# Optimization experiments

Measured on AMD Instinct MI355X. Metric: run time of the kernel, lower is better.

The kernel has to match this reference:

```python
import jax, jax.numpy as jnp
import numpy as np

K = 8            # hard-coded knn k
NS = 0.2         # LeakyReLU negative slope
EPS = 1e-6
LN_EPS = 1e-5
H = 6            # num_heads


def vn_lin(W, x):
    # VNLinear: linear over vector-channel dim (axis 1). x: (B, Cin, 3, ...)
    return jnp.einsum('oc,bc...->bo...', W, x)


def vn_leaky(x, W, U):
    # VNLinearLeakyReLU (no BN): feature map p, direction map d
    p = vn_lin(W, x)
    d = vn_lin(U, x)
    dot = jnp.sum(p * d, axis=2, keepdims=True)
    dsq = jnp.sum(d * d, axis=2, keepdims=True)
    neg = p - (dot / (dsq + EPS)) * d
    return NS * p + (1.0 - NS) * jnp.where(dot >= 0, p, neg)


def vn_layernorm(x, g, b):
    # LayerNorm on per-channel vector norms, rescale directions. x: (B,C,3,N)
    n = jnp.sqrt(jnp.sum(x * x, axis=2) + EPS)            # (B,C,N)
    mu = jnp.mean(n, axis=1, keepdims=True)
    var = jnp.var(n, axis=1, keepdims=True)
    nhat = (n - mu) / jnp.sqrt(var + LN_EPS)
    nnew = g[None, :, None] * nhat + b[None, :, None]
    return x * (nnew / n)[:, :, None, :]


def vn_attention(vn_x, Wq, Wk, Wv, Wo):
    # vn_x: (B, C, 3, N); VNLinear(C, 3C) projections, multi-head SDPA over N
    B, C, _, N = vn_x.shape
    def heads(W):
        t = vn_lin(W, vn_x)                               # (B, 3C, 3, N)
        t = t.reshape(B, H, 3 * C // H, 3, N)
        return t.transpose(0, 1, 4, 2, 3).reshape(B, H, N, -1)  # (B,H,N,9C/H)
    q, k, v = heads(Wq), heads(Wk), heads(Wv)
    scale = (3 * C // H) ** -0.5                          # head_dim = dim//H = 64
    attn = jax.nn.softmax(jnp.einsum('bhqd,bhkd->bhqk', q, k) * scale, axis=-1)
    o = jnp.einsum('bhqk,bhkd->bhqd', attn, v)            # (B,H,N,9C/H)
    o = o.transpose(0, 2, 1, 3).reshape(B, N, 3 * C, 3).transpose(0, 2, 3, 1)
    return vn_lin(Wo, o)                                  # (B, C, 3, N)


def vn_get_graph_feature(x, knn_index):
    # x: (B, C, 3, N); knn_index: flat (B*K*N,) into (B*N) rows
    B, C, _, N = x.shape
    xp = x.transpose(0, 3, 1, 2).reshape(B * N, C * 3)
    feat = xp[knn_index].reshape(B, K, N, C, 3)
    xc = x.transpose(0, 3, 1, 2).reshape(B, 1, N, C, 3)
    f = jnp.concatenate([feat - xc, jnp.broadcast_to(xc, (B, K, N, C, 3))], axis=3)
    return f.transpose(0, 3, 4, 2, 1)                     # (B, 2C, 3, N, K)


def setup_inputs() -> dict:
    key = jax.random.key(0)
    ks = jax.random.split(key, 20)
    B, N, C = 4, 2048, 128
    def w(k, o, i):
        return jax.random.normal(k, (o, i), jnp.float32) * (i ** -0.5)
    return {
        'x': jax.random.normal(ks[0], (B, N, 3 * C), jnp.float32),
        'knn_index': jax.random.randint(ks[1], (B * K * N,), 0, B * N),
        'g1': jnp.ones((C,), jnp.float32), 'b1': jnp.zeros((C,), jnp.float32),
        'g2': jnp.ones((C,), jnp.float32), 'b2': jnp.zeros((C,), jnp.float32),
        'Wq': w(ks[2], 3 * C, C), 'Wk': w(ks[3], 3 * C, C), 'Wv': w(ks[4], 3 * C, C),
        'Wo': w(ks[5], C, 3 * C),
        'W1': w(ks[6], C, 2 * C), 'U1': w(ks[7], C, 2 * C),   # conv1: 256->128
        'W2': w(ks[8], C, 2 * C),                               # conv2: 256->128
        'W3': w(ks[9], 2 * C, C), 'U3': w(ks[10], 2 * C, C),   # conv3: 128->256
        'W4': w(ks[11], C, 2 * C), 'U4': w(ks[12], C, 2 * C),  # conv4: 256->128
    }


def reference(x, knn_index, g1, b1, g2, b2, Wq, Wk, Wv, Wo, W1, U1, W2, W3, U3, W4, U4):
    B, N, D = x.shape
    C = D // 3
    vn_x = x.transpose(0, 2, 1).reshape(B, C, 3, N)
    norm_x = vn_layernorm(vn_x, g1, b1)
    x_1 = vn_attention(norm_x, Wq, Wk, Wv, Wo)            # (B,C,3,N)
    knn_f = vn_get_graph_feature(norm_x, knn_index)       # (B,2C,3,N,K)
    knn_f = vn_leaky(knn_f, W1, U1)                       # (B,C,3,N,K)
    knn_f = jnp.mean(knn_f, axis=-1)                      # mean_pool over k
    x_1 = jnp.concatenate([x_1, knn_f], axis=1)           # (B,2C,3,N)
    x_1 = vn_lin(W2, x_1)                                 # (B,C,3,N)
    vn_x = vn_x + x_1
    nx2 = vn_layernorm(vn_x, g2, b2)
    h = vn_leaky(nx2, W3, U3)                             # (B,2C,3,N)
    h = vn_leaky(h, W4, U4)                               # (B,C,3,N)
    vn_x = vn_x + h
    return vn_x.reshape(B, D, N).transpose(0, 2, 1)       # (B,N,384)
```

## Files before the change

kernel.cpp:

```cpp
#include <hip/hip_runtime.h>
#include <math.h>

#define NFIX 2048
#define HH 6
#define KNN 8
#define NSLOPE 0.2f
#define EPSF 1e-6f
#define LNEPSF 1e-5f
#define QSCALE 0.18033688011112042f
#define NSPLIT 2

typedef unsigned short ushort_t;
typedef unsigned int uint_t;
typedef __attribute__((ext_vector_type(8))) short bf16x8;
typedef __attribute__((ext_vector_type(4))) short bf16x4;
typedef __attribute__((ext_vector_type(8))) _Float16 f16x8;
typedef __attribute__((ext_vector_type(4))) _Float16 f16x4;
typedef __attribute__((ext_vector_type(16))) float f32x16;
typedef __attribute__((ext_vector_type(4))) float f32x4;

__device__ __forceinline__ ushort_t f2bf(float f) {
  union { float f; unsigned u; } v; v.f = f;
  unsigned r = v.u + 0x7fff + ((v.u >> 16) & 1);
  return (ushort_t)(r >> 16);
}
__device__ __forceinline__ float bf2f(ushort_t u) {
  union { uint_t u; float f; } v; v.u = ((uint_t)u) << 16; return v.f;
}
__device__ __forceinline__ uint_t pack2(float a, float b) {
  return (uint_t)f2bf(a) | ((uint_t)f2bf(b) << 16);
}
__device__ __forceinline__ ushort_t f2h_bits(float a) {
  union { _Float16 h; ushort_t s; } cv; cv.h = (_Float16)a; return cv.s;
}
__device__ __forceinline__ uint_t packh2(float a, float b) {
  union { _Float16 h; ushort_t s; } ha, hb;
  ha.h = (_Float16)a; hb.h = (_Float16)b;
  return (uint_t)ha.s | ((uint_t)hb.s << 16);
}

__device__ __forceinline__ void vnleaky3(const float* p, const float* dv, float* out) {
  float dot = p[0]*dv[0] + p[1]*dv[1] + p[2]*dv[2];
  float dsq = dv[0]*dv[0] + dv[1]*dv[1] + dv[2]*dv[2] + EPSF;
  float f = dot / dsq;
#pragma unroll
  for (int d = 0; d < 3; ++d) {
    float neg = p[d] - f * dv[d];
    out[d] = NSLOPE * p[d] + (1.f - NSLOPE) * ((dot >= 0.f) ? p[d] : neg);
  }
}

__global__ __launch_bounds__(256) void prep_ln1(
    const float* __restrict__ Wq, const float* __restrict__ Wk,
    const float* __restrict__ Wv, const float* __restrict__ Wo,
    const float* __restrict__ W1, const float* __restrict__ U1,
    const float* __restrict__ W2, const float* __restrict__ W3,
    const float* __restrict__ U3, const float* __restrict__ W4,
    const float* __restrict__ U4,
    ushort_t* __restrict__ Wall, _Float16* __restrict__ Af16,
    _Float16* __restrict__ W3h, _Float16* __restrict__ U3h,
    _Float16* __restrict__ W4h, _Float16* __restrict__ U4h,
    const float* __restrict__ xin, ushort_t* __restrict__ xbp,
    float* __restrict__ xdi, const float* __restrict__ g1,
    const float* __restrict__ b1) {
  __shared__ float red[8];
  int bi = blockIdx.x;
  if (bi >= 1600) {
    int t = threadIdx.x;
    int half = t >> 7, c = t & 127;
    int bn = (bi - 1600) * 2 + half;
    const float* row = xin + (size_t)bn * 384;
    float x0 = row[c*3+0], x1 = row[c*3+1], x2 = row[c*3+2];
    float nv = sqrtf(x0*x0 + x1*x1 + x2*x2 + EPSF);
    float s1 = nv, s2 = nv*nv;
#pragma unroll
    for (int off = 32; off >= 1; off >>= 1) {
      s1 += __shfl_down(s1, off);
      s2 += __shfl_down(s2, off);
    }
    int lane = t & 63, w = t >> 6;
    if (lane == 0) { red[w*2] = s1; red[w*2+1] = s2; }
    __syncthreads();
    int rb4 = (w >> 1) * 4;
    float tot1 = red[rb4] + red[rb4+2], tot2 = red[rb4+1] + red[rb4+3];
    float mu  = tot1 * (1.f/128.f);
    float var = tot2 * (1.f/128.f) - mu*mu;
    float rsig = rsqrtf(var + LNEPSF);
    float nnew = g1[c] * ((nv - mu) * rsig) + b1[c];
    float sc = nnew / nv;
    size_t rb = (size_t)bn * 384;
    xbp[rb + c]       = f2bf(x0*sc);
    xbp[rb + 128 + c] = f2bf(x1*sc);
    xbp[rb + 256 + c] = f2bf(x2*sc);
    xdi[rb + c]       = x0;
    xdi[rb + 128 + c] = x1;
    xdi[rb + 256 + c] = x2;
    return;
  }
  int idx = bi * 256 + threadIdx.x;
  if (idx < 212992) {
    int m = idx >> 7, c = idx & 127;
    float val;
    if (m < 384)       val = Wq[m*128 + c] * QSCALE;
    else if (m < 768)  val = Wk[(m-384)*128 + c];
    else if (m < 1152) val = Wv[(m-768)*128 + c];
    else {
      int j = m - 1152;
      if (j < 128)      val = W1[j*256 + c];
      else if (j < 256) val = U1[(j-128)*256 + c];
      else if (j < 384) { int o = j-256; val = W1[o*256 + 128 + c] - W1[o*256 + c]; }
      else              { int o = j-384; val = U1[o*256 + 128 + c] - U1[o*256 + c]; }
    }
    Wall[idx] = f2bf(val); return;
  }
  idx -= 212992;
  if (idx < 49152) {
    int c = idx / 384, j = idx % 384;
    float s = 0.f;
    for (int cp = 0; cp < 128; ++cp) s += W2[c*256 + cp] * Wo[cp*384 + j];
    Af16[(size_t)c*512 + j] = (_Float16)s; return;
  }
  idx -= 49152;
  if (idx < 16384) {
    int c2 = idx / 128, c = idx % 128;
    Af16[(size_t)c*512 + 384 + c2] = (_Float16)W2[c*256 + 128 + c2]; return;
  }
  idx -= 16384;
  if (idx < 32768) { W3h[idx] = (_Float16)W3[idx]; return; }
  idx -= 32768;
  if (idx < 32768) { U3h[idx] = (_Float16)U3[idx]; return; }
  idx -= 32768;
  if (idx < 32768) { W4h[idx] = (_Float16)W4[idx]; return; }
  idx -= 32768;
  if (idx < 32768) { U4h[idx] = (_Float16)U4[idx]; return; }
}

#define XT_PITCH 132
#define WT_PITCH 132
#define TR_PITCH 36
__global__ __launch_bounds__(256, 2) void qkv_conv1_mfma(
    const ushort_t* __restrict__ xb, const ushort_t* __restrict__ Wall,
    ushort_t* __restrict__ q, ushort_t* __restrict__ k, ushort_t* __restrict__ v,
    _Float16* __restrict__ YZh, _Float16* __restrict__ NBh) {
  __shared__ ushort_t xs[128*XT_PITCH];
  __shared__ ushort_t wt[32*WT_PITCH];
  __shared__ float tr[4][32*TR_PITCH];
  int nb = blockIdx.x % 192;
  int mq = blockIdx.x / 192;
  int n0 = nb * 128;
  int t = threadIdx.x;
  int w = t >> 6, lane = t & 63, ql = lane & 31, hl = lane >> 5;
  for (int idx = t; idx < 2048; idx += 256) {
    int n = idx >> 4, c16 = idx & 15;
    bf16x8 gv = *(const bf16x8*)&xb[(size_t)(n0 + n)*128 + c16*8];
    ushort_t* dst = &xs[n*XT_PITCH + c16*8];
    *(bf16x4*)dst = __builtin_shufflevector(gv, gv, 0, 1, 2, 3);
    *(bf16x4*)(dst+4) = __builtin_shufflevector(gv, gv, 4, 5, 6, 7);
  }
  __syncthreads();
  bf16x8 xf[8];
  {
    const ushort_t* xr = &xs[(w*32 + ql)*XT_PITCH + hl*8];
#pragma unroll
    for (int cs = 0; cs < 8; ++cs) {
      bf16x4 lo = *(const bf16x4*)(xr + cs*16);
      bf16x4 hi = *(const bf16x4*)(xr + cs*16 + 4);
      xf[cs] = __builtin_shufflevector(lo, hi, 0, 1, 2, 3, 4, 5, 6, 7);
    }
  }
  int ng = n0 + w*32 + ql;
  int pt = ng / 3;
  int d  = ng - 3*pt;
  float* trw = tr[w];
  for (int mt = 0; mt < 13; ++mt) {
    int m0 = mq*416 + mt*32;
    __syncthreads();
    for (int idx = t; idx < 512; idx += 256) {
      int mm = idx >> 4, c16 = idx & 15;
      bf16x8 gv = *(const bf16x8*)&Wall[(size_t)(m0 + mm)*128 + c16*8];
      ushort_t* dst = &wt[mm*WT_PITCH + c16*8];
      *(bf16x4*)dst = __builtin_shufflevector(gv, gv, 0, 1, 2, 3);
      *(bf16x4*)(dst+4) = __builtin_shufflevector(gv, gv, 4, 5, 6, 7);
    }
    __syncthreads();
    f32x16 acc;
#pragma unroll
    for (int r = 0; r < 16; ++r) acc[r] = 0.f;
    const ushort_t* wr = &wt[ql*WT_PITCH + hl*8];
#pragma unroll
    for (int cs = 0; cs < 8; ++cs) {
      bf16x4 lo = *(const bf16x4*)(wr + cs*16);
      bf16x4 hi = *(const bf16x4*)(wr + cs*16 + 4);
      bf16x8 af = __builtin_shufflevector(lo, hi, 0, 1, 2, 3, 4, 5, 6, 7);
      acc = __builtin_amdgcn_mfma_f32_32x32x16_bf16(af, xf[cs], acc, 0, 0, 0);
    }
#pragma unroll
    for (int r = 0; r < 16; ++r) {
      int mrow = (r&3) + 8*(r>>2) + 4*hl;
      trw[ql*TR_PITCH + mrow] = acc[r];
    }
    asm volatile("s_waitcnt lgkmcnt(0)" ::: "memory");
    float4 c0 = *(float4*)&trw[ql*TR_PITCH + hl*16 + 0];
    float4 c1 = *(float4*)&trw[ql*TR_PITCH + hl*16 + 4];
    float4 c2 = *(float4*)&trw[ql*TR_PITCH + hl*16 + 8];
    float4 c3 = *(float4*)&trw[ql*TR_PITCH + hl*16 + 12];
    asm volatile("s_waitcnt lgkmcnt(0)" ::: "memory");
    int mg = m0 + hl*16;
    if (m0 < 1152) {
      uint4 s0, s1;
      s0.x = pack2(c0.x, c0.y); s0.y = pack2(c0.z, c0.w);
      s0.z = pack2(c1.x, c1.y); s0.w = pack2(c1.z, c1.w);
      s1.x = pack2(c2.x, c2.y); s1.y = pack2(c2.z, c2.w);
      s1.z = pack2(c3.x, c3.y); s1.w = pack2(c3.z, c3.w);
      ushort_t* dst;
      if (m0 < 384)       dst = q + (size_t)pt*1152 + d*384 + mg;
      else if (m0 < 768)  dst = k + (size_t)pt*1152 + d*384 + (mg - 384);
      else                dst = v + (size_t)pt*1152 + d*384 + (mg - 768);
      *(uint4*)dst = s0;
      *(uint4*)(dst + 8) = s1;
    } else {
      int mat = mg - 1152;
      int sub = mat >> 7, o = mat & 127;
      _Float16* basep = (sub < 2) ? YZh : NBh;
      _Float16* dst = basep + (size_t)pt*768 + d*256 + (sub & 1)*128 + o;
      uint4 s0, s1;
      s0.x = packh2(c0.x, c0.y); s0.y = packh2(c0.z, c0.w);
      s0.z = packh2(c1.x, c1.y); s0.w = packh2(c1.z, c1.w);
      s1.x = packh2(c2.x, c2.y); s1.y = packh2(c2.z, c2.w);
      s1.z = packh2(c3.x, c3.y); s1.w = packh2(c3.z, c3.w);
      *(uint4*)dst = s0;
      *(uint4*)(dst + 8) = s1;
    }
  }
}

#define VT_LP 196
__global__ __launch_bounds__(256) void post_vtrans(const ushort_t* __restrict__ v,
    ushort_t* __restrict__ vT, const _Float16* __restrict__ YZh,
    const _Float16* __restrict__ NBh, const int* __restrict__ knn_index,
    _Float16* __restrict__ kmf16) {
  __shared__ ushort_t tl[64*VT_LP];
  __shared__ int sidx[8][KNN];
  int blk = blockIdx.x;
  int t = threadIdx.x;
  if (blk < 768) {
    int bh = blk / 32, ptile = blk % 32;
    int b = bh / HH, h = bh % HH;
    int pt0 = ptile * 64;
#pragma unroll
    for (int i = 0; i < 6; ++i) {
      int u = i*256 + t;
      int p = u / 24, seg = u % 24;
      int d = seg >> 3, c8 = seg & 7;
      bf16x8 gv = *(const bf16x8*)&v[(size_t)(b*NFIX + pt0 + p)*1152 + d*384 + h*64 + c8*8];
      ushort_t* dst = &tl[p*VT_LP + d*64 + c8*8];
      *(bf16x4*)dst = __builtin_shufflevector(gv, gv, 0, 1, 2, 3);
      *(bf16x4*)(dst+4) = __builtin_shufflevector(gv, gv, 4, 5, 6, 7);
    }
    __syncthreads();
#pragma unroll
    for (int i = 0; i < 6; ++i) {
      int u = i*256 + t;
      int ch = u >> 3, pc = u & 7;
      int ol = ch / 3, dd = ch - 3*ol;
      int cloc = dd*64 + ol;
      ushort_t hv[8];
#pragma unroll
      for (int e = 0; e < 8; ++e)
        hv[e] = tl[(pc*8 + e)*VT_LP + cloc];
      uint4 o4;
      o4.x = (uint_t)hv[0] | ((uint_t)hv[1] << 16);
      o4.y = (uint_t)hv[2] | ((uint_t)hv[3] << 16);
      o4.z = (uint_t)hv[4] | ((uint_t)hv[5] << 16);
      o4.w = (uint_t)hv[6] | ((uint_t)hv[7] << 16);
      *(uint4*)&vT[((size_t)bh*192 + ch)*2048 + pt0 + pc*8] = o4;
    }
    return;
  }
  int bnb = (blk - 768) * 8;
  int half = t >> 7, c = t & 127;
  if (t < 64) {
    int pi = t >> 3, kk = t & 7;
    int bn = bnb + pi;
    int b = bn / NFIX, n = bn % NFIX;
    sidx[pi][kk] = knn_index[(b*KNN + kk)*NFIX + n];
  }
  __syncthreads();
#pragma unroll
  for (int pi2 = 0; pi2 < 4; ++pi2) {
    int pi = half*4 + pi2;
    int bn = bnb + pi;
    float yb[3], zb[3];
#pragma unroll
    for (int d = 0; d < 3; ++d) {
      yb[d] = (float)NBh[(size_t)bn*768 + d*256 + c];
      zb[d] = (float)NBh[(size_t)bn*768 + d*256 + 128 + c];
    }
    float om[3] = {0.f, 0.f, 0.f};
#pragma unroll
    for (int kk = 0; kk < KNN; ++kk) {
      const _Float16* r = YZh + (size_t)sidx[pi][kk]*768;
      float p[3], dd[3];
#pragma unroll
      for (int d = 0; d < 3; ++d) {
        p[d]  = (float)r[d*256 + c] + yb[d];
        dd[d] = (float)r[d*256 + 128 + c] + zb[d];
      }
      float res[3];
      vnleaky3(p, dd, res);
      om[0] += res[0]; om[1] += res[1]; om[2] += res[2];
    }
#pragma unroll
    for (int d = 0; d < 3; ++d)
      kmf16[((size_t)bn*3 + d)*128 + c] = (_Float16)(om[d] * (1.f/KNN));
  }
}

#define KT_P 196
#define VT_P 36
#define TW_P 195
__global__ __launch_bounds__(256, 2) void attn_kernel(const ushort_t* __restrict__ q,
    const ushort_t* __restrict__ k, const ushort_t* __restrict__ vT,
    ushort_t* __restrict__ opart, float* __restrict__ lpart) {
  __shared__ ushort_t kt[2][32*KT_P];
  __shared__ ushort_t vt[2][192*VT_P];
  __shared__ float alds[4][32];
  int blk = blockIdx.x;
  int xcd = blk & 7, j = blk >> 3;
  int g = xcd*6 + (j >> 4);
  int qt = j & 15;
  int bh = g % 24;
  int split = g / 24;
  int b = bh / HH, h = bh % HH;
  int t = threadIdx.x;
  int w = t >> 6, lane = t & 63, ql = lane & 31, hl = lane >> 5;
  int qrow0 = qt*128 + w*32;
  const ushort_t* qpb = q + (size_t)(b*NFIX + qrow0 + ql)*1152 + h*64;
  bf16x8 qf[12];
#pragma unroll
  for (int cs = 0; cs < 12; ++cs) {
    int red0 = cs*16 + hl*8;
    int dq = red0 >> 6, ml = red0 & 63;
    qf[cs] = *(const bf16x8*)(qpb + dq*384 + ml);
  }
  const ushort_t* ksrc[3]; int kdsto[3];
  const ushort_t* vsrc[3]; int vdsto[3];
#pragma unroll
  for (int j2 = 0; j2 < 3; ++j2) {
    int idx = t + j2*256;
    int kp = idx / 24, c16 = idx % 24;
    int red0 = c16*8;
    int dk = red0 >> 6, ml = red0 & 63;
    ksrc[j2] = k + (size_t)(b*NFIX + kp)*1152 + dk*384 + h*64 + ml;
    kdsto[j2] = kp*KT_P + c16*8;
    int ch = idx >> 2, c4 = idx & 3;
    vsrc[j2] = vT + ((size_t)bh*192 + ch)*2048 + c4*8;
    vdsto[j2] = ch*VT_P + c4*8;
  }
  f32x16 acc[6];
#pragma unroll
  for (int nt = 0; nt < 6; ++nt)
#pragma unroll
    for (int r = 0; r < 16; ++r) acc[nt][r] = 0.f;
  float lsum = 0.f;
  int koff0 = split * 1024;
  bf16x8 kpre[3], vpre[3];
#pragma unroll
  for (int j2 = 0; j2 < 3; ++j2) {
    kpre[j2] = *(const bf16x8*)(ksrc[j2] + (size_t)koff0*1152);
    vpre[j2] = *(const bf16x8*)(vsrc[j2] + koff0);
  }
#pragma unroll
  for (int j2 = 0; j2 < 3; ++j2) {
    ushort_t* kd = &kt[0][kdsto[j2]];
    *(bf16x4*)kd = __builtin_shufflevector(kpre[j2], kpre[j2], 0, 1, 2, 3);
    *(bf16x4*)(kd+4) = __builtin_shufflevector(kpre[j2], kpre[j2], 4, 5, 6, 7);
    ushort_t* vd = &vt[0][vdsto[j2]];
    *(bf16x4*)vd = __builtin_shufflevector(vpre[j2], vpre[j2], 0, 1, 2, 3);
    *(bf16x4*)(vd+4) = __builtin_shufflevector(vpre[j2], vpre[j2], 4, 5, 6, 7);
  }
  __syncthreads();
  for (int kb = 0; kb < 32; ++kb) {
    int cur = kb & 1;
    if (kb < 31) {
      int koff = koff0 + (kb+1)*32;
#pragma unroll
      for (int j2 = 0; j2 < 3; ++j2) {
        kpre[j2] = *(const bf16x8*)(ksrc[j2] + (size_t)koff*1152);
        vpre[j2] = *(const bf16x8*)(vsrc[j2] + koff);
      }
    }
    f32x16 sca, scb;
#pragma unroll
    for (int r = 0; r < 16; ++r) { sca[r] = 0.f; scb[r] = 0.f; }
    const ushort_t* ktc = kt[cur];
#pragma unroll
    for (int cs = 0; cs < 12; ++cs) {
      const ushort_t* kr = &ktc[ql*KT_P + cs*16 + hl*8];
      bf16x4 alo = *(const bf16x4*)kr;
      bf16x4 ahi = *(const bf16x4*)(kr + 4);
      bf16x8 af = __builtin_shufflevector(alo, ahi, 0, 1, 2, 3, 4, 5, 6, 7);
      if (cs & 1) scb = __builtin_amdgcn_mfma_f32_32x32x16_bf16(af, qf[cs], scb, 0, 0, 0);
      else        sca = __builtin_amdgcn_mfma_f32_32x32x16_bf16(af, qf[cs], sca, 0, 0, 0);
    }
    uint_t u[8], pex[8];
#pragma unroll
    for (int g2 = 0; g2 < 4; ++g2) {
      float p0 = __builtin_amdgcn_exp2f(sca[g2*4 + 0] + scb[g2*4 + 0]);
      float p1 = __builtin_amdgcn_exp2f(sca[g2*4 + 1] + scb[g2*4 + 1]);
      float p2 = __builtin_amdgcn_exp2f(sca[g2*4 + 2] + scb[g2*4 + 2]);
      float p3 = __builtin_amdgcn_exp2f(sca[g2*4 + 3] + scb[g2*4 + 3]);
      lsum += (p0 + p1) + (p2 + p3);
      u[2*g2]   = pack2(p0, p1);
      u[2*g2+1] = pack2(p2, p3);
    }
#pragma unroll
    for (int j2 = 0; j2 < 8; ++j2) pex[j2] = (uint_t)__shfl_xor((int)u[j2], 32);
    const ushort_t* vtc = vt[cur];
#pragma unroll
    for (int s = 0; s < 2; ++s) {
      uint4 au;
      au.x = hl ? pex[4*s+2] : u[4*s+0];
      au.y = hl ? pex[4*s+3] : u[4*s+1];
      au.z = hl ? u[4*s+2]   : pex[4*s+0];
      au.w = hl ? u[4*s+3]   : pex[4*s+1];
      union { uint4 ui; bf16x8 bv; } cvt; cvt.ui = au;
      bf16x8 pa = cvt.bv;
#pragma unroll
      for (int nt = 0; nt < 6; ++nt) {
        const ushort_t* vr = &vtc[(nt*32 + ql)*VT_P + s*16 + hl*8];
        bf16x4 vlo = *(const bf16x4*)vr;
        bf16x4 vhi = *(const bf16x4*)(vr + 4);
        bf16x8 vf = __builtin_shufflevector(vlo, vhi, 0, 1, 2, 3, 4, 5, 6, 7);
        acc[nt] = __builtin_amdgcn_mfma_f32_32x32x16_bf16(pa, vf, acc[nt], 0, 0, 0);
      }
    }
    if (kb < 31) {
      int nxt = cur ^ 1;
#pragma unroll
      for (int j2 = 0; j2 < 3; ++j2) {
        ushort_t* kd = &kt[nxt][kdsto[j2]];
        *(bf16x4*)kd = __builtin_shufflevector(kpre[j2], kpre[j2], 0, 1, 2, 3);
        *(bf16x4*)(kd+4) = __builtin_shufflevector(kpre[j2], kpre[j2], 4, 5, 6, 7);
        ushort_t* vd = &vt[nxt][vdsto[j2]];
        *(bf16x4*)vd = __builtin_shufflevector(vpre[j2], vpre[j2], 0, 1, 2, 3);
        *(bf16x4*)(vd+4) = __builtin_shufflevector(vpre[j2], vpre[j2], 4, 5, 6, 7);
      }
    }
    __syncthreads();
  }
  lsum += __shfl_xor(lsum, 32);
  if (lane < 32) {
    alds[w][ql] = 1.0f / lsum;
    lpart[(size_t)split*24*NFIX + (size_t)bh*NFIX + qrow0 + ql] = lsum;
  }
  asm volatile("s_waitcnt lgkmcnt(0)" ::: "memory");
  float lv[4][4];
#pragma unroll
  for (int g2 = 0; g2 < 4; ++g2) {
    f32x4 tv = *(const f32x4*)&alds[w][8*g2 + 4*hl];
#pragma unroll
    for (int rr = 0; rr < 4; ++rr) lv[g2][rr] = tv[rr];
  }
  ushort_t* tw = (w == 0) ? kt[0] : (w == 1) ? kt[1] : (w == 2) ? vt[0] : vt[1];
#pragma unroll
  for (int nt = 0; nt < 6; ++nt) {
    int ch = nt*32 + ql;
#pragma unroll
    for (int r = 0; r < 16; ++r) {
      int qrow = (r&3) + 8*(r>>2) + 4*hl;
      tw[qrow*TW_P + ch] = f2h_bits(acc[nt][r] * lv[r>>2][r&3]);
    }
  }
  asm volatile("s_waitcnt lgkmcnt(0)" ::: "memory");
  const size_t SS = (size_t)8192*1152;
  ushort_t* opb = opart + (size_t)split*SS;
  size_t nbase = (size_t)(b*NFIX + qrow0) * 3;
#pragma unroll
  for (int i = 0; i < 12; ++i) {
    int chunk = i*64 + lane;
    int nl = chunk >> 3, jc = chunk & 7;
    int qq = nl / 3, dd = nl - 3*qq;
    ushort_t hv[8];
#pragma unroll
    for (int e = 0; e < 8; ++e)
      hv[e] = tw[qq*TW_P + (jc*8 + e)*3 + dd];
    uint4 sv;
    sv.x = (uint_t)hv[0] | ((uint_t)hv[1] << 16);
    sv.y = (uint_t)hv[2] | ((uint_t)hv[3] << 16);
    sv.z = (uint_t)hv[4] | ((uint_t)hv[5] << 16);
    sv.w = (uint_t)hv[6] | ((uint_t)hv[7] << 16);
    *(uint4*)&opb[(nbase + nl)*384 + h*64 + jc*8] = sv;
  }
}

#define AP 68
#define XLP 132
__global__ __launch_bounds__(768) void x1mid_mfma(
    const float* __restrict__ xdi, const ushort_t* __restrict__ opart,
    const float* __restrict__ lpart, const _Float16* __restrict__ kmf16,
    const _Float16* __restrict__ Af16, float* __restrict__ xmid,
    _Float16* __restrict__ nxh, const float* __restrict__ g2,
    const float* __restrict__ b2) {
  __shared__ __align__(16) char smem[50944];
  _Float16* As = (_Float16*)smem;
  _Float16* Bt = (_Float16*)(smem + 17408);
  float* wlsL  = (float*)(smem + 30464);
  float* X     = (float*)smem;
  float* stats = (float*)(smem + 50688);
  int blk = blockIdx.x;
  int n0 = blk * 96;
  int pt0 = blk * 32;
  int t = threadIdx.x;
  int w = t >> 6, lane = t & 63, ql = lane & 31, hl = lane >> 5;
  int nsub = w >> 2, mt2 = w & 3;
  if (t < 192) {
    int ptl = t / 6, h = t % 6;
    int ptg = pt0 + ptl;
    int b = ptg >> 11, n = ptg & 2047;
    size_t lidx = (size_t)(b*HH + h)*NFIX + n;
    float l[NSPLIT]; float tot = 0.f;
#pragma unroll
    for (int s = 0; s < NSPLIT; ++s) {
      l[s] = lpart[(size_t)s*24*NFIX + lidx];
      tot += l[s];
    }
    float rd = 1.f / tot;
    float* wp = &wlsL[(ptl*6 + h)*NSPLIT];
#pragma unroll
    for (int s = 0; s < NSPLIT; ++s) wp[s] = l[s]*rd;
  }
  f32x16 acc;
#pragma unroll
  for (int r = 0; r < 16; ++r) acc[r] = 0.f;
  const size_t SS = (size_t)8192*1152;
  __syncthreads();
  for (int p = 0; p < 8; ++p) {
    for (int u = t; u < 1024; u += 768) {
      int m = u >> 3, kc = u & 7;
      f16x4 a0 = *(const f16x4*)&Af16[(size_t)m*512 + p*64 + kc*8];
      f16x4 a1 = *(const f16x4*)&Af16[(size_t)m*512 + p*64 + kc*8 + 4];
      _Float16* dst = &As[m*AP + kc*8];
      *(f16x4*)dst = a0;
      *(f16x4*)(dst+4) = a1;
    }
    {
      int n_l = t >> 3, jc = t & 7;
      int n_g = n0 + n_l;
      _Float16* dst = &Bt[n_l*AP + jc*8];
      if (p < 6) {
        int pt_l = n_l / 3;
        const float* wp = &wlsL[(pt_l*6 + p)*NSPLIT];
        float facc[8];
#pragma unroll
        for (int e = 0; e < 8; ++e) facc[e] = 0.f;
#pragma unroll
        for (int s = 0; s < NSPLIT; ++s) {
          const ushort_t* src = opart + s*SS + (size_t)n_g*384 + p*64 + jc*8;
          uint4 ra = *(const uint4*)src;
          const _Float16* ua = (const _Float16*)&ra;
          float wsc = wp[s];
#pragma unroll
          for (int e = 0; e < 8; ++e)
            facc[e] += wsc * (float)ua[e];
        }
        _Float16 hv[8];
#pragma unroll
        for (int e = 0; e < 8; ++e) hv[e] = (_Float16)facc[e];
        *(f16x4*)dst = *(f16x4*)&hv[0];
        *(f16x4*)(dst+4) = *(f16x4*)&hv[4];
      } else {
        const _Float16* src = kmf16 + (size_t)n_g*128 + (p-6)*64 + jc*8;
        f16x4 v0 = *(const f16x4*)src;
        f16x4 v1 = *(const f16x4*)(src + 4);
        *(f16x4*)dst = v0; *(f16x4*)(dst+4) = v1;
      }
    }
    __syncthreads();
#pragma unroll
    for (int cs = 0; cs < 4; ++cs) {
      int kloc = cs*16 + hl*8;
      f16x4 b0 = *(const f16x4*)&Bt[(nsub*32 + ql)*AP + kloc];
      f16x4 b1 = *(const f16x4*)&Bt[(nsub*32 + ql)*AP + kloc + 4];
      f16x8 bf = __builtin_shufflevector(b0, b1, 0, 1, 2, 3, 4, 5, 6, 7);
      int mrow = mt2*32 + ql;
      f16x4 a0 = *(const f16x4*)&As[mrow*AP + kloc];
      f16x4 a1 = *(const f16x4*)&As[mrow*AP + kloc + 4];
      f16x8 af = __builtin_shufflevector(a0, a1, 0, 1, 2, 3, 4, 5, 6, 7);
      acc = __builtin_amdgcn_mfma_f32_32x32x16_f16(af, bf, acc, 0, 0, 0);
    }
    __syncthreads();
  }
  {
    int cbase = mt2*32 + 4*hl;
    float* xrow = &X[(nsub*32 + ql)*XLP];
#pragma unroll
    for (int r = 0; r < 16; ++r) {
      int col = cbase + (r&3) + 8*(r>>2);
      xrow[col] = acc[r];
    }
  }
  __syncthreads();
#pragma unroll
  for (int i = 0; i < 2; ++i) {
    int u = i*768 + t;
    int row = u >> 4, c0 = (u & 15) * 8;
    float* xp = &X[row*XLP + c0];
    const float* xd = xdi + (size_t)(n0 + row)*128 + c0;
    float4 a0 = *(float4*)xp, a1 = *(float4*)(xp + 4);
    float4 d0 = *(const float4*)xd, d1 = *(const float4*)(xd + 4);
    a0.x += d0.x; a0.y += d0.y; a0.z += d0.z; a0.w += d0.w;
    a1.x += d1.x; a1.y += d1.y; a1.z += d1.z; a1.w += d1.w;
    *(float4*)xp = a0; *(float4*)(xp + 4) = a1;
    float* dst = xmid + (size_t)(n0 + row)*128 + c0;
    *(float4*)dst = a0; *(float4*)(dst + 4) = a1;
  }
  __syncthreads();
  for (int pi = w; pi < 32; pi += 12) {
    int c = lane;
    float a0 = X[(pi*3+0)*XLP + c], a1 = X[(pi*3+1)*XLP + c], a2 = X[(pi*3+2)*XLP + c];
    float e0 = X[(pi*3+0)*XLP + c + 64], e1 = X[(pi*3+1)*XLP + c + 64], e2 = X[(pi*3+2)*XLP + c + 64];
    float nva = sqrtf(a0*a0 + a1*a1 + a2*a2 + EPSF);
    float nvb = sqrtf(e0*e0 + e1*e1 + e2*e2 + EPSF);
    float s1 = nva + nvb;
    float s2 = nva*nva + nvb*nvb;
#pragma unroll
    for (int off = 32; off >= 1; off >>= 1) {
      s1 += __shfl_down(s1, off);
      s2 += __shfl_down(s2, off);
    }
    if (lane == 0) {
      float mu = s1 * (1.f/128.f);
      float var = s2 * (1.f/128.f) - mu*mu;
      stats[pi*2]   = mu;
      stats[pi*2+1] = rsqrtf(var + LNEPSF);
    }
  }
  __syncthreads();
#pragma unroll
  for (int i = 0; i < 2; ++i) {
    int u = i*768 + t;
    int row = u >> 4, c0 = (u & 15) * 8;
    int pt_l = row / 3;
    float mu = stats[pt_l*2], rsig = stats[pt_l*2+1];
    const float* r0 = &X[(pt_l*3 + 0)*XLP + c0];
    const float* r1 = &X[(pt_l*3 + 1)*XLP + c0];
    const float* r2 = &X[(pt_l*3 + 2)*XLP + c0];
    const float* rd = &X[row*XLP + c0];
    float xv[8];
#pragma unroll
    for (int e = 0; e < 8; ++e) {
      float x0 = r0[e], x1 = r1[e], x2 = r2[e];
      float nv = sqrtf(x0*x0 + x1*x1 + x2*x2 + EPSF);
      float nnew = g2[c0 + e] * ((nv - mu) * rsig) + b2[c0 + e];
      xv[e] = rd[e] * (nnew / nv);
    }
    uint4 sv;
    sv.x = packh2(xv[0], xv[1]); sv.y = packh2(xv[2], xv[3]);
    sv.z = packh2(xv[4], xv[5]); sv.w = packh2(xv[6], xv[7]);
    *(uint4*)&nxh[(size_t)(n0 + row)*128 + c0] = sv;
  }
}

#define X3P 132
#define TR3P 36
__global__ __launch_bounds__(256) void conv3_mfma(const _Float16* __restrict__ nxh,
    const _Float16* __restrict__ W3h, const _Float16* __restrict__ U3h,
    _Float16* __restrict__ h3) {
  __shared__ __align__(16) _Float16 Xs[3*32*X3P];
  __shared__ __align__(16) _Float16 tr3[4][96*TR3P];
  int blk = blockIdx.x;
  int pt0 = (blk >> 1) * 32;
  int oh = blk & 1;
  int t = threadIdx.x;
  int w = t >> 6, lane = t & 63, ql = lane & 31, hl = lane >> 5;
#pragma unroll
  for (int i = 0; i < 6; ++i) {
    int u = i*256 + t;
    int r = u >> 4, c8 = u & 15;
    f16x8 gv = *(const f16x8*)&nxh[(size_t)(pt0*3 + r)*128 + c8*8];
    int d = r % 3, p = r / 3;
    _Float16* dst = &Xs[(d*32 + p)*X3P + c8*8];
    *(f16x4*)dst = __builtin_shufflevector(gv, gv, 0, 1, 2, 3);
    *(f16x4*)(dst+4) = __builtin_shufflevector(gv, gv, 4, 5, 6, 7);
  }
  __syncthreads();
  int ot = oh*128 + w*32;
  const _Float16* Wp = W3h + (size_t)(ot + ql)*128 + hl*8;
  const _Float16* Up = U3h + (size_t)(ot + ql)*128 + hl*8;
  f32x16 accP[3], accD[3];
#pragma unroll
  for (int d = 0; d < 3; ++d)
#pragma unroll
    for (int r = 0; r < 16; ++r) { accP[d][r] = 0.f; accD[d][r] = 0.f; }
#pragma unroll
  for (int cs = 0; cs < 8; ++cs) {
    f16x8 wf = *(const f16x8*)(Wp + cs*16);
    f16x8 uf = *(const f16x8*)(Up + cs*16);
#pragma unroll
    for (int d = 0; d < 3; ++d) {
      const _Float16* xr = &Xs[(d*32 + ql)*X3P + cs*16 + hl*8];
      f16x4 lo = *(const f16x4*)xr;
      f16x4 hi = *(const f16x4*)(xr + 4);
      f16x8 xf = __builtin_shufflevector(lo, hi, 0, 1, 2, 3, 4, 5, 6, 7);
      accP[d] = __builtin_amdgcn_mfma_f32_32x32x16_f16(wf, xf, accP[d], 0, 0, 0);
      accD[d] = __builtin_amdgcn_mfma_f32_32x32x16_f16(uf, xf, accD[d], 0, 0, 0);
    }
  }
  _Float16* trw = tr3[w];
#pragma unroll
  for (int r = 0; r < 16; ++r) {
    int olr = (r&3) + 8*(r>>2) + 4*hl;
    float p3[3], d3[3], res[3];
#pragma unroll
    for (int d = 0; d < 3; ++d) { p3[d] = accP[d][r]; d3[d] = accD[d][r]; }
    vnleaky3(p3, d3, res);
#pragma unroll
    for (int d = 0; d < 3; ++d) trw[(ql*3 + d)*TR3P + olr] = (_Float16)res[d];
  }
  asm volatile("s_waitcnt lgkmcnt(0)" ::: "memory");
#pragma unroll
  for (int i = 0; i < 6; ++i) {
    int u = i*64 + lane;
    int row = u >> 2, c8 = u & 3;
    const _Float16* src = &trw[row*TR3P + c8*8];
    f16x4 lo = *(const f16x4*)src;
    f16x4 hi = *(const f16x4*)(src + 4);
    f16x8 ov = __builtin_shufflevector(lo, hi, 0, 1, 2, 3, 4, 5, 6, 7);
    *(f16x8*)&h3[(size_t)(pt0*3 + row)*256 + ot + c8*8] = ov;
  }
}

#define X4P 260
#define TF4P 388
__global__ __launch_bounds__(256) void conv4_mfma(const _Float16* __restrict__ h3,
    const _Float16* __restrict__ W4h, const _Float16* __restrict__ U4h,
    const float* __restrict__ xmid, float* __restrict__ out) {
  __shared__ __align__(16) _Float16 Xs[3*16*X4P];
  __shared__ __align__(16) float trF[16*TF4P];
  int pt0 = blockIdx.x * 16;
  int t = threadIdx.x;
  int w = t >> 6, lane = t & 63;
  int nl = lane & 15, kq = lane >> 4;
#pragma unroll
  for (int i = 0; i < 6; ++i) {
    int u = i*256 + t;
    int r = u >> 5, c8 = u & 31;
    f16x8 gv = *(const f16x8*)&h3[(size_t)(pt0*3 + r)*256 + c8*8];
    int d = r % 3, p = r / 3;
    _Float16* dst = &Xs[(d*16 + p)*X4P + c8*8];
    *(f16x4*)dst = __builtin_shufflevector(gv, gv, 0, 1, 2, 3);
    *(f16x4*)(dst+4) = __builtin_shufflevector(gv, gv, 4, 5, 6, 7);
  }
  __syncthreads();
  int ot = w*32;
  f32x4 accP[2][3], accD[2][3];
#pragma unroll
  for (int mt = 0; mt < 2; ++mt)
#pragma unroll
    for (int d = 0; d < 3; ++d)
#pragma unroll
      for (int r = 0; r < 4; ++r) { accP[mt][d][r] = 0.f; accD[mt][d][r] = 0.f; }
  const _Float16* Wb = W4h + (size_t)ot*256;
  const _Float16* Ub = U4h + (size_t)ot*256;
#pragma unroll
  for (int cs = 0; cs < 8; ++cs) {
    int kof = cs*32 + kq*8;
    f16x8 xf[3];
#pragma unroll
    for (int d = 0; d < 3; ++d) {
      const _Float16* xr = &Xs[(d*16 + nl)*X4P + kof];
      f16x4 lo = *(const f16x4*)xr;
      f16x4 hi = *(const f16x4*)(xr + 4);
      xf[d] = __builtin_shufflevector(lo, hi, 0, 1, 2, 3, 4, 5, 6, 7);
    }
#pragma unroll
    for (int mt = 0; mt < 2; ++mt) {
      f16x8 wf = *(const f16x8*)(Wb + (size_t)(mt*16 + nl)*256 + kof);
      f16x8 uf = *(const f16x8*)(Ub + (size_t)(mt*16 + nl)*256 + kof);
#pragma unroll
      for (int d = 0; d < 3; ++d) {
        accP[mt][d] = __builtin_amdgcn_mfma_f32_16x16x32_f16(wf, xf[d], accP[mt][d], 0, 0, 0);
        accD[mt][d] = __builtin_amdgcn_mfma_f32_16x16x32_f16(uf, xf[d], accD[mt][d], 0, 0, 0);
      }
    }
  }
#pragma unroll
  for (int mt = 0; mt < 2; ++mt)
#pragma unroll
    for (int r = 0; r < 4; ++r) {
      int o = ot + mt*16 + kq*4 + r;
      float p3[3], d3[3], res[3];
#pragma unroll
      for (int d = 0; d < 3; ++d) { p3[d] = accP[mt][d][r]; d3[d] = accD[mt][d][r]; }
      vnleaky3(p3, d3, res);
#pragma unroll
      for (int d = 0; d < 3; ++d) trF[nl*TF4P + o*3 + d] = res[d];
    }
  __syncthreads();
#pragma unroll
  for (int i = 0; i < 6; ++i) {
    int u = i*256 + t;
    int row = u / 96, c4 = u % 96;
    float4 vv = *(float4*)&trF[row*TF4P + c4*4];
    int bn = pt0 + row;
    float rs[4];
    const float* fv = (const float*)&vv;
#pragma unroll
    for (int e = 0; e < 4; ++e) {
      int col = c4*4 + e;
      int o = col / 3, d = col - 3*o;
      rs[e] = fv[e] + xmid[(size_t)(3*bn + d)*128 + o];
    }
    float4 ov; ov.x = rs[0]; ov.y = rs[1]; ov.z = rs[2]; ov.w = rs[3];
    *(float4*)&out[(size_t)bn*384 + c4*4] = ov;
  }
}

extern "C" void kernel_launch(void* const* d_in, const int* in_sizes, int n_in,
                              void* d_out, int out_size, void* d_ws, size_t ws_size,
                              hipStream_t stream) {
  const float* x   = (const float*)d_in[0];
  const int* knn   = (const int*)d_in[1];
  const float* g1  = (const float*)d_in[2];
  const float* b1  = (const float*)d_in[3];
  const float* g2  = (const float*)d_in[4];
  const float* b2  = (const float*)d_in[5];
  const float* Wq  = (const float*)d_in[6];
  const float* Wk  = (const float*)d_in[7];
  const float* Wv  = (const float*)d_in[8];
  const float* Wo  = (const float*)d_in[9];
  const float* W1  = (const float*)d_in[10];
  const float* U1  = (const float*)d_in[11];
  const float* W2  = (const float*)d_in[12];
  const float* W3  = (const float*)d_in[13];
  const float* U3  = (const float*)d_in[14];
  const float* W4  = (const float*)d_in[15];
  const float* U4  = (const float*)d_in[16];
  float* out = (float*)d_out;
  (void)n_in; (void)out_size; (void)ws_size;

  const size_t BN = (size_t)in_sizes[0] / 384;

  float* ws    = (float*)d_ws;
  float* xdi   = ws;
  float* xmid  = xdi + BN*384;
  _Float16* kmf16 = (_Float16*)(xmid + BN*384);
  ushort_t* xbp = (ushort_t*)(kmf16 + BN*384);
  ushort_t* qb = xbp + BN*384;
  ushort_t* kb = qb + BN*1152;
  ushort_t* vb = kb + BN*1152;
  ushort_t* vT = vb + BN*1152;
  ushort_t* Wall = vT + BN*1152;
  _Float16* Af16 = (_Float16*)(Wall + 212992);
  _Float16* W3h = Af16 + 65536;
  _Float16* U3h = W3h + 32768;
  _Float16* W4h = U3h + 32768;
  _Float16* U4h = W4h + 32768;
  ushort_t* opart = (ushort_t*)(U4h + 32768);
  float* lpart = (float*)(opart + 4*BN*1152);
  _Float16* YZh = (_Float16*)opart;
  _Float16* NBh = YZh + BN*768;
  _Float16* nxh = (_Float16*)qb;
  _Float16* h3  = (_Float16*)kb;

  prep_ln1<<<1600 + 4096, 256, 0, stream>>>(Wq, Wk, Wv, Wo, W1, U1, W2, W3, U3, W4, U4,
                                            Wall, Af16, W3h, U3h, W4h, U4h,
                                            x, xbp, xdi, g1, b1);
  qkv_conv1_mfma<<<192*4, 256, 0, stream>>>(xbp, Wall, qb, kb, vb, YZh, NBh);
  post_vtrans<<<768 + 1024, 256, 0, stream>>>(vb, vT, YZh, NBh, knn, kmf16);
  attn_kernel<<<16*24*NSPLIT, 256, 0, stream>>>(qb, kb, vT, opart, lpart);
  x1mid_mfma<<<256, 768, 0, stream>>>(xdi, opart, lpart, kmf16, Af16, xmid, nxh, g2, b2);
  conv3_mfma<<<512, 256, 0, stream>>>(nxh, W3h, U3h, h3);
  conv4_mfma<<<512, 256, 0, stream>>>(h3, W4h, U4h, xmid, out);
}
```

Before: 316.0 us.

## Fuse conv3 and conv4 into one kernel keeping hidden activations in LDS

Merges the conv3 and conv4 VN-leaky layers into one 512-thread kernel that processes 32 points per block. The 256-channel hidden result stays in shared memory instead of going through the global h3 buffer, which removes one launch and the h3 write and re-read. Shared memory is reused across the stages with extra barriers. The cost is fewer blocks (256 instead of 512), so occupancy and parallelism drop.

```diff
diff --git a/kernel.cpp b/kernel.cpp
--- a/kernel.cpp
+++ b/kernel.cpp
@@ -663,31 +663,33 @@
 }
 
 #define X3P 132
-#define TR3P 36
-__global__ __launch_bounds__(256) void conv3_mfma(const _Float16* __restrict__ nxh,
+#define HP4 260
+#define TF4P 388
+__global__ __launch_bounds__(512) void conv34_fused(const _Float16* __restrict__ nxh,
     const _Float16* __restrict__ W3h, const _Float16* __restrict__ U3h,
-    _Float16* __restrict__ h3) {
-  __shared__ __align__(16) _Float16 Xs[3*32*X3P];
-  __shared__ __align__(16) _Float16 tr3[4][96*TR3P];
-  int blk = blockIdx.x;
-  int pt0 = (blk >> 1) * 32;
-  int oh = blk & 1;
+    const _Float16* __restrict__ W4h, const _Float16* __restrict__ U4h,
+    const float* __restrict__ xmid, float* __restrict__ out) {
+  __shared__ __align__(16) char smem[49920];
+  _Float16* Xs3 = (_Float16*)smem;
+  _Float16* H   = (_Float16*)smem;
+  float* trF    = (float*)smem;
+  int pt0 = blockIdx.x * 32;
   int t = threadIdx.x;
   int w = t >> 6, lane = t & 63, ql = lane & 31, hl = lane >> 5;
 #pragma unroll
-  for (int i = 0; i < 6; ++i) {
-    int u = i*256 + t;
+  for (int i = 0; i < 3; ++i) {
+    int u = i*512 + t;
     int r = u >> 4, c8 = u & 15;
     f16x8 gv = *(const f16x8*)&nxh[(size_t)(pt0*3 + r)*128 + c8*8];
     int d = r % 3, p = r / 3;
-    _Float16* dst = &Xs[(d*32 + p)*X3P + c8*8];
+    _Float16* dst = &Xs3[(d*32 + p)*X3P + c8*8];
     *(f16x4*)dst = __builtin_shufflevector(gv, gv, 0, 1, 2, 3);
     *(f16x4*)(dst+4) = __builtin_shufflevector(gv, gv, 4, 5, 6, 7);
   }
   __syncthreads();
-  int ot = oh*128 + w*32;
-  const _Float16* Wp = W3h + (size_t)(ot + ql)*128 + hl*8;
-  const _Float16* Up = U3h + (size_t)(ot + ql)*128 + hl*8;
+  int ot3 = w*32;
+  const _Float16* Wp = W3h + (size_t)(ot3 + ql)*128 + hl*8;
+  const _Float16* Up = U3h + (size_t)(ot3 + ql)*128 + hl*8;
   f32x16 accP[3], accD[3];
 #pragma unroll
   for (int d = 0; d < 3; ++d)
@@ -699,7 +701,7 @@
     f16x8 uf = *(const f16x8*)(Up + cs*16);
 #pragma unroll
     for (int d = 0; d < 3; ++d) {
-      const _Float16* xr = &Xs[(d*32 + ql)*X3P + cs*16 + hl*8];
+      const _Float16* xr = &Xs3[(d*32 + ql)*X3P + cs*16 + hl*8];
       f16x4 lo = *(const f16x4*)xr;
       f16x4 hi = *(const f16x4*)(xr + 4);
       f16x8 xf = __builtin_shufflevector(lo, hi, 0, 1, 2, 3, 4, 5, 6, 7);
@@ -707,7 +709,7 @@
       accD[d] = __builtin_amdgcn_mfma_f32_32x32x16_f16(uf, xf, accD[d], 0, 0, 0);
     }
   }
-  _Float16* trw = tr3[w];
+  __syncthreads();
 #pragma unroll
   for (int r = 0; r < 16; ++r) {
     int olr = (r&3) + 8*(r>>2) + 4*hl;
@@ -716,60 +718,29 @@
     for (int d = 0; d < 3; ++d) { p3[d] = accP[d][r]; d3[d] = accD[d][r]; }
     vnleaky3(p3, d3, res);
 #pragma unroll
-    for (int d = 0; d < 3; ++d) trw[(ql*3 + d)*TR3P + olr] = (_Float16)res[d];
-  }
-  asm volatile("s_waitcnt lgkmcnt(0)" ::: "memory");
-#pragma unroll
-  for (int i = 0; i < 6; ++i) {
-    int u = i*64 + lane;
-    int row = u >> 2, c8 = u & 3;
-    const _Float16* src = &trw[row*TR3P + c8*8];
-    f16x4 lo = *(const f16x4*)src;
-    f16x4 hi = *(const f16x4*)(src + 4);
-    f16x8 ov = __builtin_shufflevector(lo, hi, 0, 1, 2, 3, 4, 5, 6, 7);
-    *(f16x8*)&h3[(size_t)(pt0*3 + row)*256 + ot + c8*8] = ov;
-  }
-}
-
-#define X4P 260
-#define TF4P 388
-__global__ __launch_bounds__(256) void conv4_mfma(const _Float16* __restrict__ h3,
-    const _Float16* __restrict__ W4h, const _Float16* __restrict__ U4h,
-    const float* __restrict__ xmid, float* __restrict__ out) {
-  __shared__ __align__(16) _Float16 Xs[3*16*X4P];
-  __shared__ __align__(16) float trF[16*TF4P];
-  int pt0 = blockIdx.x * 16;
-  int t = threadIdx.x;
-  int w = t >> 6, lane = t & 63;
+    for (int d = 0; d < 3; ++d)
+      H[(d*32 + ql)*HP4 + ot3 + olr] = (_Float16)res[d];
+  }
+  __syncthreads();
+  int ph = w >> 2;
+  int ot4 = (w & 3) * 32;
   int nl = lane & 15, kq = lane >> 4;
-#pragma unroll
-  for (int i = 0; i < 6; ++i) {
-    int u = i*256 + t;
-    int r = u >> 5, c8 = u & 31;
-    f16x8 gv = *(const f16x8*)&h3[(size_t)(pt0*3 + r)*256 + c8*8];
-    int d = r % 3, p = r / 3;
-    _Float16* dst = &Xs[(d*16 + p)*X4P + c8*8];
-    *(f16x4*)dst = __builtin_shufflevector(gv, gv, 0, 1, 2, 3);
-    *(f16x4*)(dst+4) = __builtin_shufflevector(gv, gv, 4, 5, 6, 7);
-  }
-  __syncthreads();
-  int ot = w*32;
-  f32x4 accP[2][3], accD[2][3];
+  f32x4 acc4P[2][3], acc4D[2][3];
 #pragma unroll
   for (int mt = 0; mt < 2; ++mt)
 #pragma unroll
     for (int d = 0; d < 3; ++d)
 #pragma unroll
-      for (int r = 0; r < 4; ++r) { accP[mt][d][r] = 0.f; accD[mt][d][r] = 0.f; }
-  const _Float16* Wb = W4h + (size_t)ot*256;
-  const _Float16* Ub = U4h + (size_t)ot*256;
+      for (int r = 0; r < 4; ++r) { acc4P[mt][d][r] = 0.f; acc4D[mt][d][r] = 0.f; }
+  const _Float16* Wb = W4h + (size_t)ot4*256;
+  const _Float16* Ub = U4h + (size_t)ot4*256;
 #pragma unroll
   for (int cs = 0; cs < 8; ++cs) {
     int kof = cs*32 + kq*8;
     f16x8 xf[3];
 #pragma unroll
     for (int d = 0; d < 3; ++d) {
-      const _Float16* xr = &Xs[(d*16 + nl)*X4P + kof];
+      const _Float16* xr = &H[(d*32 + ph*16 + nl)*HP4 + kof];
       f16x4 lo = *(const f16x4*)xr;
       f16x4 hi = *(const f16x4*)(xr + 4);
       xf[d] = __builtin_shufflevector(lo, hi, 0, 1, 2, 3, 4, 5, 6, 7);
@@ -780,27 +751,29 @@
       f16x8 uf = *(const f16x8*)(Ub + (size_t)(mt*16 + nl)*256 + kof);
 #pragma unroll
       for (int d = 0; d < 3; ++d) {
-        accP[mt][d] = __builtin_amdgcn_mfma_f32_16x16x32_f16(wf, xf[d], accP[mt][d], 0, 0, 0);
-        accD[mt][d] = __builtin_amdgcn_mfma_f32_16x16x32_f16(uf, xf[d], accD[mt][d], 0, 0, 0);
+        acc4P[mt][d] = __builtin_amdgcn_mfma_f32_16x16x32_f16(wf, xf[d], acc4P[mt][d], 0, 0, 0);
+        acc4D[mt][d] = __builtin_amdgcn_mfma_f32_16x16x32_f16(uf, xf[d], acc4D[mt][d], 0, 0, 0);
       }
     }
   }
+  __syncthreads();
 #pragma unroll
   for (int mt = 0; mt < 2; ++mt)
 #pragma unroll
     for (int r = 0; r < 4; ++r) {
-      int o = ot + mt*16 + kq*4 + r;
+      int o = ot4 + mt*16 + kq*4 + r;
+      int p_l = ph*16 + nl;
       float p3[3], d3[3], res[3];
 #pragma unroll
-      for (int d = 0; d < 3; ++d) { p3[d] = accP[mt][d][r]; d3[d] = accD[mt][d][r]; }
+      for (int d = 0; d < 3; ++d) { p3[d] = acc4P[mt][d][r]; d3[d] = acc4D[mt][d][r]; }
       vnleaky3(p3, d3, res);
 #pragma unroll
-      for (int d = 0; d < 3; ++d) trF[nl*TF4P + o*3 + d] = res[d];
+      for (int d = 0; d < 3; ++d) trF[p_l*TF4P + o*3 + d] = res[d];
     }
   __syncthreads();
 #pragma unroll
   for (int i = 0; i < 6; ++i) {
-    int u = i*256 + t;
+    int u = i*512 + t;
     int row = u / 96, c4 = u % 96;
     float4 vv = *(float4*)&trF[row*TF4P + c4*4];
     int bn = pt0 + row;
@@ -862,7 +835,6 @@
   _Float16* YZh = (_Float16*)opart;
   _Float16* NBh = YZh + BN*768;
   _Float16* nxh = (_Float16*)qb;
-  _Float16* h3  = (_Float16*)kb;
 
   prep_ln1<<<1600 + 4096, 256, 0, stream>>>(Wq, Wk, Wv, Wo, W1, U1, W2, W3, U3, W4, U4,
                                             Wall, Af16, W3h, U3h, W4h, U4h,
@@ -871,6 +843,5 @@
   post_vtrans<<<768 + 1024, 256, 0, stream>>>(vb, vT, YZh, NBh, knn, kmf16);
   attn_kernel<<<16*24*NSPLIT, 256, 0, stream>>>(qb, kb, vT, opart, lpart);
   x1mid_mfma<<<256, 768, 0, stream>>>(xdi, opart, lpart, kmf16, Af16, xmid, nxh, g2, b2);
-  conv3_mfma<<<512, 256, 0, stream>>>(nxh, W3h, U3h, h3);
-  conv4_mfma<<<512, 256, 0, stream>>>(h3, W4h, U4h, xmid, out);
-}
+  conv34_fused<<<256, 512, 0, stream>>>(nxh, W3h, U3h, W4h, U4h, xmid, out);
+}
```

Result: no change. 312.3 us (-1.2%).
